# Performance work log

Measured on AMD Instinct MI355X. Metric: run time of the kernel, lower is better.

## Reference

```python
import jax, jax.numpy as jnp
import numpy as np
from jax import lax

EPS = 1e-5  # BatchNorm eps (inference-style BN with running stats)


def _bn(x, g, b, m, v):
    scale = g / jnp.sqrt(v + EPS)
    return x * scale[None, :, None, None] + (b - m * scale)[None, :, None, None]


def _conv1x1_bn(x, w, g, b, m, v):
    # ConvNormActivation(in_ch, out, k=1, activation=None) -> 1x1 conv (no bias) + BN
    y = jnp.einsum('bchw,oc->bohw', x, w)
    return _bn(y, g, b, m, v)


def _upsample_bilinear_ac(x, scale):
    # nn.Upsample(scale_factor=scale, mode='bilinear', align_corners=True)
    B, C, H, W = x.shape
    Ho, Wo = H * scale, W * scale

    def coords(n_in, n_out):
        s = jnp.arange(n_out, dtype=x.dtype) * ((n_in - 1) / (n_out - 1))
        i0 = jnp.clip(jnp.floor(s).astype(jnp.int32), 0, n_in - 2)
        t = s - i0.astype(x.dtype)
        return i0, t

    iy, ty = coords(H, Ho)
    ix, tx = coords(W, Wo)
    x = x[:, :, iy, :] * (1 - ty)[None, None, :, None] + x[:, :, iy + 1, :] * ty[None, None, :, None]
    x = x[:, :, :, ix] * (1 - tx) + x[:, :, :, ix + 1] * tx
    return x


def _dcnv2(x, off_w, off_b, w):
    # DCNv2: internal 3x3 conv -> 18 offsets (dy,dx per tap) + 9 sigmoid masks,
    # then modulated deformable 3x3 conv (stride 1, pad 1, no bias).
    B, C, H, W = x.shape
    K2 = 9
    om = lax.conv_general_dilated(x, off_w, (1, 1), ((1, 1), (1, 1)),
                                  dimension_numbers=('NCHW', 'OIHW', 'NCHW'))
    om = om + off_b[None, :, None, None]
    off = om[:, :2 * K2].reshape(B, K2, 2, H, W)          # (dy, dx) per kernel tap
    mask = jax.nn.sigmoid(om[:, 2 * K2:3 * K2])           # [B,9,H,W]

    ky, kx = jnp.meshgrid(jnp.arange(3), jnp.arange(3), indexing='ij')
    base_y = (jnp.arange(H)[None, :, None] + (ky.reshape(K2) - 1)[:, None, None]).astype(x.dtype)  # [9,H,1]
    base_x = (jnp.arange(W)[None, None, :] + (kx.reshape(K2) - 1)[:, None, None]).astype(x.dtype)  # [9,1,W]
    sy = base_y[None] + off[:, :, 0]                      # [B,9,H,W]
    sx = base_x[None] + off[:, :, 1]

    xf = x.reshape(B, C, H * W)
    y0 = jnp.floor(sy)
    x0 = jnp.floor(sx)
    val = jnp.zeros((B, C, K2, H, W), x.dtype)
    for dy in (0, 1):
        for dx in (0, 1):
            yy = y0 + dy
            xx = x0 + dx
            wgt = (1 - jnp.abs(sy - yy)) * (1 - jnp.abs(sx - xx))
            valid = (yy >= 0) & (yy <= H - 1) & (xx >= 0) & (xx <= W - 1)
            idx = jnp.clip(yy, 0, H - 1).astype(jnp.int32) * W + jnp.clip(xx, 0, W - 1).astype(jnp.int32)
            g = jnp.take_along_axis(xf, idx.reshape(B, 1, -1), axis=2).reshape(B, C, K2, H, W)
            val = val + g * (wgt * valid.astype(x.dtype))[:, None]
    val = val * mask[:, None]
    return jnp.einsum('bckhw,ock->bohw', val, w.reshape(w.shape[0], C, K2))


def _forward(f0, f1, f2, f3,
             w0, g0, b0, m0, v0, w1, g1, b1, m1, v1,
             w2, g2, b2, m2, v2, w3, g3, b3, m3, v3,
             off_w, off_b, dcn_w, gf, bf, mf, vf):
    x1 = _conv1x1_bn(f0, w0, g0, b0, m0, v0)
    x2 = _upsample_bilinear_ac(_conv1x1_bn(f1, w1, g1, b1, m1, v1), 2)
    x3 = _upsample_bilinear_ac(_conv1x1_bn(f2, w2, g2, b2, m2, v2), 4)
    x4 = _upsample_bilinear_ac(_conv1x1_bn(f3, w3, g3, b3, m3, v3), 8)
    x = jax.nn.relu(x1 + x2 + x3 + x4)
    y = _dcnv2(x, off_w, off_b, dcn_w)
    return jax.nn.relu(_bn(y, gf, bf, mf, vf))


def setup_inputs() -> dict:
    key = jax.random.key(0)
    ks = iter(jax.random.split(key, 64))

    def rn(shape, scale=1.0):
        return jax.random.normal(next(ks), shape, dtype=jnp.float32) * scale

    def ru(shape):
        return jax.random.uniform(next(ks), shape, dtype=jnp.float32)

    C = 64
    inp = {}
    inp['f0'] = rn((4, 64, 160, 160))
    inp['f1'] = rn((4, 128, 80, 80))
    inp['f2'] = rn((4, 256, 40, 40))
    inp['f3'] = rn((4, 512, 20, 20))
    for i, cin in enumerate([64, 128, 256, 512]):
        inp[f'w{i}'] = rn((C, cin), 1.0 / np.sqrt(cin))
        inp[f'g{i}'] = rn((C,))
        inp[f'b{i}'] = rn((C,))
        inp[f'm{i}'] = rn((C,))
        inp[f'v{i}'] = ru((C,))
    inp['off_w'] = rn((27, C, 3, 3), 0.01)   # small offsets, like post-training DCN
    inp['off_b'] = rn((27,), 0.01)
    inp['dcn_w'] = rn((C, C, 3, 3), 1.0 / np.sqrt(C * 9))
    inp['gf'] = rn((C,))
    inp['bf'] = rn((C,))
    inp['mf'] = rn((C,))
    inp['vf'] = ru((C,))
    return inp


def reference(f0, f1, f2, f3,
              w0, g0, b0, m0, v0, w1, g1, b1, m1, v1,
              w2, g2, b2, m2, v2, w3, g3, b3, m3, v3,
              off_w, off_b, dcn_w, gf, bf, mf, vf):
    return _forward(f0, f1, f2, f3,
                    w0, g0, b0, m0, v0, w1, g1, b1, m1, v1,
                    w2, g2, b2, m2, v2, w3, g3, b3, m3, v3,
                    off_w, off_b, dcn_w, gf, bf, mf, vf)
```

## Files before the change

kernel.cpp:

```cpp
#include <hip/hip_runtime.h>
#include <math.h>

#define EPSB 1e-5f

constexpr int B_ = 4;
constexpr int C_ = 64;
constexpr int H_ = 160;
constexpr int W_ = 160;
constexpr int HW_ = H_ * W_;

constexpr size_t X_OFF   = 0;
constexpr size_t Y1_OFF  = X_OFF  + (size_t)B_ * HW_ * 64;
constexpr size_t Y2_OFF  = Y1_OFF + (size_t)B_ * 6400 * 64;
constexpr size_t Y3_OFF  = Y2_OFF + (size_t)B_ * 1600 * 64;
constexpr size_t OM_OFF  = Y3_OFF + (size_t)B_ * 400 * 64;
constexpr size_t WR0_OFF = OM_OFF + (size_t)B_ * HW_ * 27;
constexpr size_t WTB_OFF = WR0_OFF + 4096;
constexpr size_t RWB_OFF = WTB_OFF + (9 * 64 * 72) / 2;
constexpr size_t SB_OFF  = RWB_OFF + (9 * 32 * 64) / 2;
constexpr size_t WR1_OFF = X_OFF + 0;
constexpr size_t WR2_OFF = X_OFF + 8192;
constexpr size_t WR3_OFF = X_OFF + 24576;

typedef short bf16x8 __attribute__((ext_vector_type(8)));
typedef float f32x4 __attribute__((ext_vector_type(4)));

static __device__ __forceinline__ unsigned short f2bf(float f) {
    unsigned int u = __float_as_uint(f);
    u += 0x7fff + ((u >> 16) & 1);
    return (unsigned short)(u >> 16);
}

__global__ __launch_bounds__(256) void prep_kernel(
    const float* __restrict__ g0, const float* __restrict__ b0, const float* __restrict__ m0, const float* __restrict__ v0,
    const float* __restrict__ g1, const float* __restrict__ b1, const float* __restrict__ m1, const float* __restrict__ v1,
    const float* __restrict__ g2, const float* __restrict__ b2, const float* __restrict__ m2, const float* __restrict__ v2,
    const float* __restrict__ g3, const float* __restrict__ b3, const float* __restrict__ m3, const float* __restrict__ v3,
    const float* __restrict__ gf, const float* __restrict__ bf, const float* __restrict__ mf, const float* __restrict__ vf,
    const float* __restrict__ w0, const float* __restrict__ w1, const float* __restrict__ w2, const float* __restrict__ w3,
    const float* __restrict__ dcn_w, const float* __restrict__ off_w,
    float* __restrict__ ws)
{
    int tid = blockIdx.x * 256 + threadIdx.x;
    if (tid < 320) {
        int j = tid >> 6, c = tid & 63;
        const float *g, *b, *m, *v;
        switch (j) {
            case 0: g = g0; b = b0; m = m0; v = v0; break;
            case 1: g = g1; b = b1; m = m1; v = v1; break;
            case 2: g = g2; b = b2; m = m2; v = v2; break;
            case 3: g = g3; b = b3; m = m3; v = v3; break;
            default: g = gf; b = bf; m = mf; v = vf; break;
        }
        float sc = g[c] * rsqrtf(v[c] + EPSB);
        ws[SB_OFF + j * 128 + c]      = sc;
        ws[SB_OFF + j * 128 + 64 + c] = b[c] - m[c] * sc;
        return;
    }
    int t = tid - 320;
    if (t < 4096) {
        int ci = t >> 6, o = t & 63;
        ws[WR0_OFF + t] = w0[o * 64 + ci];
        return;
    }
    t -= 4096;
    if (t < 9 * 64 * 72) {
        int k = t / 4608, r = t % 4608, o = r / 72, c = r % 72;
        float v = (c < 64) ? dcn_w[o * 576 + c * 9 + k] : 0.f;
        ((unsigned short*)(ws + WTB_OFF))[t] = f2bf(v);
        return;
    }
    t -= 9 * 64 * 72;
    if (t < 9 * 32 * 64) {
        int tap = t >> 11, r = t & 2047, o = r >> 6, ci = r & 63;
        float v = (o < 27) ? off_w[o * 576 + ci * 9 + tap] : 0.f;
        ((unsigned short*)(ws + RWB_OFF))[t] = f2bf(v);
        return;
    }
    t -= 9 * 32 * 64;
    if (t < 8192) {
        int ci = t >> 6, o = t & 63;
        ws[WR1_OFF + t] = w1[o * 128 + ci];
        return;
    }
    t -= 8192;
    if (t < 16384) {
        int ci = t >> 6, o = t & 63;
        ws[WR2_OFF + t] = w2[o * 256 + ci];
        return;
    }
    t -= 16384;
    if (t < 32768) {
        int ci = t >> 6, o = t & 63;
        ws[WR3_OFF + t] = w3[o * 512 + ci];
        return;
    }
}

__global__ __launch_bounds__(256) void conv_all_kernel(
    const float* __restrict__ f1in, const float* __restrict__ f2in, const float* __restrict__ f3in,
    float* __restrict__ ws)
{
    __shared__ float R0[64 * 65];
    __shared__ float R1[64 * 65];
    __shared__ float SBl[128];

    int blk = blockIdx.x;
    const float* fin; const float* wr; const float* sbg; float* yout;
    int Cin, hw, tile;
    if (blk < 400)      { fin = f1in; wr = ws + WR1_OFF; sbg = ws + SB_OFF + 128; yout = ws + Y1_OFF; Cin = 128; hw = 6400; tile = blk; }
    else if (blk < 500) { fin = f2in; wr = ws + WR2_OFF; sbg = ws + SB_OFF + 256; yout = ws + Y2_OFF; Cin = 256; hw = 1600; tile = blk - 400; }
    else                { fin = f3in; wr = ws + WR3_OFF; sbg = ws + SB_OFF + 384; yout = ws + Y3_OFF; Cin = 512; hw = 400;  tile = blk - 500; }

    int tid  = threadIdx.x;
    int lane = tid & 63;
    int wv   = __builtin_amdgcn_readfirstlane(tid >> 6);

    if (tid < 128) SBl[tid] = sbg[tid];

    int P = tile * 64 + lane;
    int b = P / hw;
    int p = P - b * hw;

    int cq = Cin >> 2;
    const float* fb = fin + ((size_t)b * Cin + (size_t)wv * cq) * hw + p;
    const float* wq = wr + (wv * cq) * 64;

    float acc[64];
#pragma unroll
    for (int o = 0; o < 64; o++) acc[o] = 0.f;

    for (int c0 = 0; c0 < cq; c0 += 8) {
        float fv[8];
#pragma unroll
        for (int j = 0; j < 8; j++) fv[j] = fb[(size_t)(c0 + j) * hw];
#pragma unroll
        for (int j = 0; j < 8; j++) {
            const float* wrow = wq + (c0 + j) * 64;
#pragma unroll
            for (int o = 0; o < 64; o++) acc[o] = fmaf(fv[j], wrow[o], acc[o]);
        }
    }

    if (wv == 2) {
#pragma unroll
        for (int o = 0; o < 64; o++) R0[lane * 65 + o] = acc[o];
    }
    if (wv == 3) {
#pragma unroll
        for (int o = 0; o < 64; o++) R1[lane * 65 + o] = acc[o];
    }
    __syncthreads();
    if (wv == 0) {
#pragma unroll
        for (int o = 0; o < 64; o++) acc[o] += R0[lane * 65 + o];
    }
    if (wv == 1) {
#pragma unroll
        for (int o = 0; o < 64; o++) acc[o] += R1[lane * 65 + o];
    }
    __syncthreads();
    if (wv == 1) {
#pragma unroll
        for (int o = 0; o < 64; o++) R0[lane * 65 + o] = acc[o];
    }
    __syncthreads();
    if (wv == 0) {
#pragma unroll
        for (int o = 0; o < 64; o++) {
            float v = acc[o] + R0[lane * 65 + o];
            R1[lane * 65 + o] = fmaf(v, SBl[o], SBl[64 + o]);
        }
    }
    __syncthreads();

#pragma unroll
    for (int it = 0; it < 16; it++) {
        int idx = it * 256 + tid;
        int px = idx >> 6, o = idx & 63;
        yout[(size_t)(tile * 64 + px) * 64 + o] = R1[px * 65 + o];
    }
}

__global__ __launch_bounds__(256) void fuse_kernel(const float* __restrict__ f0, float* __restrict__ ws)
{
    __shared__ float Ot[64 * 68];

    int tid = threadIdx.x;
    int blk = blockIdx.x;
    int xcd = blk & 7, slot = blk >> 3;
    int b = xcd >> 1;
    int t = (xcd & 1) * 200 + slot;
    int p0 = t * 64;
    int lane = tid & 63;
    int cb = __builtin_amdgcn_readfirstlane(tid >> 6);
    int p = p0 + lane;
    const float* wr0 = ws + WR0_OFF + cb * 16;
    const float* sb  = ws + SB_OFF;

    {
        float acc[16];
#pragma unroll
        for (int i = 0; i < 16; i++) acc[i] = 0.f;

        const float* f0b = f0 + (size_t)b * 64 * HW_ + p;
        for (int ci0 = 0; ci0 < 64; ci0 += 8) {
            float fv[8];
#pragma unroll
            for (int j = 0; j < 8; j++) fv[j] = f0b[(size_t)(ci0 + j) * HW_];
#pragma unroll
            for (int j = 0; j < 8; j++) {
                const float* wrow = wr0 + (ci0 + j) * 64;
#pragma unroll
                for (int i = 0; i < 16; i++) acc[i] = fmaf(fv[j], wrow[i], acc[i]);
            }
        }
        float* orow = Ot + lane * 68 + cb * 16;
#pragma unroll
        for (int i = 0; i < 16; i++) {
            int o = cb * 16 + i;
            orow[i] = fmaf(acc[i], sb[o], sb[64 + o]);
        }
    }
    __syncthreads();

    {
        int chunk = lane & 15, pxo = lane >> 4;
        float* xb = ws + X_OFF + ((size_t)b * HW_ + p0) * 64;
#pragma unroll
        for (int r = 0; r < 4; r++) {
            int gpx = cb * 16 + r * 4 + pxo;
            int gp = p0 + gpx;
            int h = gp / W_, w = gp % W_;

            float fy1 = h * (79.f / 159.f); int i1 = (int)fy1; if (i1 > 78) i1 = 78; float ty1 = fy1 - i1;
            float fx1 = w * (79.f / 159.f); int j1 = (int)fx1; if (j1 > 78) j1 = 78; float tx1 = fx1 - j1;
            const float* y1 = ws + Y1_OFF + ((size_t)b * 6400 + (size_t)(i1 * 80 + j1)) * 64 + chunk * 4;
            float fy2 = h * (39.f / 159.f); int i2 = (int)fy2; if (i2 > 38) i2 = 38; float ty2 = fy2 - i2;
            float fx2 = w * (39.f / 159.f); int j2 = (int)fx2; if (j2 > 38) j2 = 38; float tx2 = fx2 - j2;
            const float* y2 = ws + Y2_OFF + ((size_t)b * 1600 + (size_t)(i2 * 40 + j2)) * 64 + chunk * 4;
            float fy3 = h * (19.f / 159.f); int i3 = (int)fy3; if (i3 > 18) i3 = 18; float ty3 = fy3 - i3;
            float fx3 = w * (19.f / 159.f); int j3 = (int)fx3; if (j3 > 18) j3 = 18; float tx3 = fx3 - j3;
            const float* y3 = ws + Y3_OFF + ((size_t)b * 400 + (size_t)(i3 * 20 + j3)) * 64 + chunk * 4;

            f32x4 A[12];
            A[0]  = *(const f32x4*)(y1);
            A[1]  = *(const f32x4*)(y1 + 64);
            A[2]  = *(const f32x4*)(y1 + 80 * 64);
            A[3]  = *(const f32x4*)(y1 + 81 * 64);
            A[4]  = *(const f32x4*)(y2);
            A[5]  = *(const f32x4*)(y2 + 64);
            A[6]  = *(const f32x4*)(y2 + 40 * 64);
            A[7]  = *(const f32x4*)(y2 + 41 * 64);
            A[8]  = *(const f32x4*)(y3);
            A[9]  = *(const f32x4*)(y3 + 64);
            A[10] = *(const f32x4*)(y3 + 20 * 64);
            A[11] = *(const f32x4*)(y3 + 21 * 64);

            f32x4 v = *(const f32x4*)(Ot + gpx * 68 + chunk * 4);

            float w00, w01, w10, w11;
            w00 = (1.f - ty1) * (1.f - tx1); w01 = (1.f - ty1) * tx1; w10 = ty1 * (1.f - tx1); w11 = ty1 * tx1;
#pragma unroll
            for (int j = 0; j < 4; j++)
                v[j] += A[0][j] * w00 + A[1][j] * w01 + A[2][j] * w10 + A[3][j] * w11;
            w00 = (1.f - ty2) * (1.f - tx2); w01 = (1.f - ty2) * tx2; w10 = ty2 * (1.f - tx2); w11 = ty2 * tx2;
#pragma unroll
            for (int j = 0; j < 4; j++)
                v[j] += A[4][j] * w00 + A[5][j] * w01 + A[6][j] * w10 + A[7][j] * w11;
            w00 = (1.f - ty3) * (1.f - tx3); w01 = (1.f - ty3) * tx3; w10 = ty3 * (1.f - tx3); w11 = ty3 * tx3;
#pragma unroll
            for (int j = 0; j < 4; j++)
                v[j] += A[8][j] * w00 + A[9][j] * w01 + A[10][j] * w10 + A[11][j] * w11;

#pragma unroll
            for (int j = 0; j < 4; j++) v[j] = fmaxf(v[j], 0.f);
            *(f32x4*)(xb + (size_t)gpx * 64 + chunk * 4) = v;
        }
    }
}

__global__ __launch_bounds__(256, 4) void dcn_fused_kernel(const float* __restrict__ off_b,
                                                           float* __restrict__ ws, float* __restrict__ out)
{
    __shared__ __align__(16) unsigned short A_lds[2][64 * 72];
    __shared__ float OMs[64 * 27];

    int tid = threadIdx.x;
    int blk = blockIdx.x;
    int xcd = blk & 7, slot = blk >> 3;
    int b = xcd >> 1;
    int t = (xcd & 1) * 200 + slot;
    int p0 = t * 64;
    int lane = tid & 63, cb = tid >> 6;
    int px = lane;
    int p = p0 + px;
    int h = p / W_, w = p % W_;
    int mrow = lane & 15, quad = lane >> 4;
    int chunk = lane & 15, pxo = lane >> 4;

    const unsigned short* rwb = (const unsigned short*)(ws + RWB_OFF);
    const unsigned short* wtb = (const unsigned short*)(ws + WTB_OFF);
    const float* xb = ws + X_OFF + (size_t)b * HW_ * 64;
    const float* sb = ws + SB_OFF + 4 * 128;

    {
        f32x4 acc2[2];
        acc2[0] = (f32x4){0.f, 0.f, 0.f, 0.f};
        acc2[1] = (f32x4){0.f, 0.f, 0.f, 0.f};

        for (int kk = 0; kk < 9; kk += 2) {
#pragma unroll
            for (int u = 0; u < 2; u++) {
                int tap = kk + u;
                if (tap > 8) break;
                int dy = tap / 3 - 1, dx = tap % 3 - 1;
                int delta = dy * W_ + dx;
                int  pss[4];
                bool vlds[4];
#pragma unroll
                for (int r = 0; r < 4; r++) {
                    int gpx = cb * 16 + r * 4 + pxo;
                    int gp = p0 + gpx;
                    int gh = gp / W_, gw = gp % W_;
                    int yy = gh + dy, xx = gw + dx;
                    vlds[r] = (yy >= 0) && (yy < H_) && (xx >= 0) && (xx < W_);
                    int ps = gp + delta;
                    pss[r] = min(max(ps, 0), HW_ - 1);
                }
                f32x4 g[4];
#pragma unroll
                for (int r = 0; r < 4; r++)
                    g[r] = *(const f32x4*)(xb + (size_t)pss[r] * 64 + chunk * 4);
#pragma unroll
                for (int r = 0; r < 4; r++) {
                    int gpx = cb * 16 + r * 4 + pxo;
                    unsigned short pk[4];
#pragma unroll
                    for (int j = 0; j < 4; j++) pk[j] = vlds[r] ? f2bf(g[r][j]) : (unsigned short)0;
                    *(unsigned int*)(A_lds[u] + gpx * 72 + chunk * 4)     = ((unsigned int)pk[1] << 16) | pk[0];
                    *(unsigned int*)(A_lds[u] + gpx * 72 + chunk * 4 + 2) = ((unsigned int)pk[3] << 16) | pk[2];
                }
            }

#pragma unroll
            for (int u = 0; u < 2; u++) {
                int tap = kk + u;
                if (tap > 8) break;
                const unsigned short* Ab = A_lds[u] + (cb * 16 + mrow) * 72;
#pragma unroll
                for (int ks = 0; ks < 2; ks++) {
                    bf16x8 af = *(const bf16x8*)(Ab + ks * 32 + quad * 8);
#pragma unroll
                    for (int nt = 0; nt < 2; nt++) {
                        bf16x8 bf_ = *(const bf16x8*)(rwb + tap * 2048 + (nt * 16 + mrow) * 64 + ks * 32 + quad * 8);
                        acc2[nt] = __builtin_amdgcn_mfma_f32_16x16x32_bf16(af, bf_, acc2[nt], 0, 0, 0);
                    }
                }
            }
        }

        __syncthreads();
        float* Cl = (float*)A_lds;
#pragma unroll
        for (int nt = 0; nt < 2; nt++) {
            int o = nt * 16 + mrow;
            if (o < 27) {
                int pr = cb * 16 + quad * 4;
#pragma unroll
                for (int r = 0; r < 4; r++) Cl[(pr + r) * 28 + o] = acc2[nt][r];
            }
        }
        __syncthreads();

        for (int k = cb; k < 9; k += 4) {
            float ady = Cl[px * 28 + 2 * k]     + off_b[2 * k];
            float adx = Cl[px * 28 + 2 * k + 1] + off_b[2 * k + 1];
            float am  = Cl[px * 28 + 18 + k]    + off_b[18 + k];
            float sy = (float)(h + k / 3 - 1) + ady;
            float sx = (float)(w + k % 3 - 1) + adx;
            float mk = 1.f / (1.f + __expf(-am));
            OMs[px * 27 + 3 * k]     = sy;
            OMs[px * 27 + 3 * k + 1] = sx;
            OMs[px * 27 + 3 * k + 2] = mk;
        }
        __syncthreads();
    }

    f32x4 acc[4];
#pragma unroll
    for (int nt = 0; nt < 4; nt++) acc[nt] = (f32x4){0.f, 0.f, 0.f, 0.f};

    for (int kk = 0; kk < 9; kk += 2) {
#pragma unroll
        for (int u = 0; u < 2; u++) {
            int k = kk + u;
            if (k > 8) break;
#pragma unroll
            for (int rp = 0; rp < 2; rp++) {
                int   idxs[2][4];
                float wvs[2][4];
#pragma unroll
                for (int rr = 0; rr < 2; rr++) {
                    int r = rp * 2 + rr;
                    int gpx = cb * 16 + r * 4 + pxo;
                    float sy = OMs[gpx * 27 + 3 * k];
                    float sx = OMs[gpx * 27 + 3 * k + 1];
                    float mk = OMs[gpx * 27 + 3 * k + 2];
                    float y0f = floorf(sy), x0f = floorf(sx);
                    int y0 = (int)y0f, x0 = (int)x0f;
                    float ty = sy - y0f, tx = sx - x0f;
#pragma unroll
                    for (int cr = 0; cr < 4; cr++) {
                        int dy = cr >> 1, dx = cr & 1;
                        int yy = y0 + dy, xx = x0 + dx;
                        float wy = dy ? ty : 1.f - ty;
                        float wx = dx ? tx : 1.f - tx;
                        bool vld = (yy >= 0) && (yy < H_) && (xx >= 0) && (xx < W_);
                        int yc = min(max(yy, 0), H_ - 1);
                        int xc = min(max(xx, 0), W_ - 1);
                        idxs[rr][cr] = yc * W_ + xc;
                        wvs[rr][cr]  = vld ? wy * wx * mk : 0.f;
                    }
                }
                f32x4 g[2][4];
#pragma unroll
                for (int rr = 0; rr < 2; rr++)
#pragma unroll
                    for (int cr = 0; cr < 4; cr++)
                        g[rr][cr] = *(const f32x4*)(xb + (size_t)idxs[rr][cr] * 64 + chunk * 4);
#pragma unroll
                for (int rr = 0; rr < 2; rr++) {
                    int r = rp * 2 + rr;
                    int gpx = cb * 16 + r * 4 + pxo;
                    f32x4 v = (f32x4){0.f, 0.f, 0.f, 0.f};
#pragma unroll
                    for (int cr = 0; cr < 4; cr++) {
                        float wv = wvs[rr][cr];
#pragma unroll
                        for (int j = 0; j < 4; j++) v[j] = fmaf(g[rr][cr][j], wv, v[j]);
                    }
                    unsigned short pk[4];
#pragma unroll
                    for (int j = 0; j < 4; j++) pk[j] = f2bf(v[j]);
                    *(unsigned int*)(A_lds[u] + gpx * 72 + chunk * 4)     = ((unsigned int)pk[1] << 16) | pk[0];
                    *(unsigned int*)(A_lds[u] + gpx * 72 + chunk * 4 + 2) = ((unsigned int)pk[3] << 16) | pk[2];
                }
            }
        }

#pragma unroll
        for (int u = 0; u < 2; u++) {
            int k = kk + u;
            if (k > 8) break;
            const unsigned short* Ab = A_lds[u] + (cb * 16 + mrow) * 72;
#pragma unroll
            for (int ks = 0; ks < 2; ks++) {
                bf16x8 af = *(const bf16x8*)(Ab + ks * 32 + quad * 8);
#pragma unroll
                for (int nt = 0; nt < 4; nt++) {
                    bf16x8 bf_ = *(const bf16x8*)(wtb + k * 4608 + (nt * 16 + mrow) * 72 + ks * 32 + quad * 8);
                    acc[nt] = __builtin_amdgcn_mfma_f32_16x16x32_bf16(af, bf_, acc[nt], 0, 0, 0);
                }
            }
        }
    }

    __syncthreads();
    float* C_lds = (float*)A_lds;
#pragma unroll
    for (int nt = 0; nt < 4; nt++) {
        int o = nt * 16 + mrow;
        int pxb = cb * 16 + quad * 4;
#pragma unroll
        for (int r = 0; r < 4; r++) C_lds[o * 65 + pxb + r] = acc[nt][r];
    }
    __syncthreads();
#pragma unroll
    for (int i = 0; i < 16; i++) {
        int o = cb * 16 + i;
        float v = C_lds[o * 65 + lane];
        v = fmaf(v, sb[o], sb[64 + o]);
        out[((size_t)b * 64 + o) * HW_ + p0 + lane] = fmaxf(v, 0.f);
    }
}

extern "C" void kernel_launch(void* const* d_in, const int* in_sizes, int n_in,
                              void* d_out, int out_size, void* d_ws, size_t ws_size,
                              hipStream_t stream)
{
    const float* f0 = (const float*)d_in[0];
    const float* f1 = (const float*)d_in[1];
    const float* f2 = (const float*)d_in[2];
    const float* f3 = (const float*)d_in[3];
    const float* w0 = (const float*)d_in[4];
    const float* g0 = (const float*)d_in[5];
    const float* b0 = (const float*)d_in[6];
    const float* m0 = (const float*)d_in[7];
    const float* v0 = (const float*)d_in[8];
    const float* w1 = (const float*)d_in[9];
    const float* g1 = (const float*)d_in[10];
    const float* b1 = (const float*)d_in[11];
    const float* m1 = (const float*)d_in[12];
    const float* v1 = (const float*)d_in[13];
    const float* w2 = (const float*)d_in[14];
    const float* g2 = (const float*)d_in[15];
    const float* b2 = (const float*)d_in[16];
    const float* m2 = (const float*)d_in[17];
    const float* v2 = (const float*)d_in[18];
    const float* w3 = (const float*)d_in[19];
    const float* g3 = (const float*)d_in[20];
    const float* b3 = (const float*)d_in[21];
    const float* m3 = (const float*)d_in[22];
    const float* v3 = (const float*)d_in[23];
    const float* off_w = (const float*)d_in[24];
    const float* off_b = (const float*)d_in[25];
    const float* dcn_w = (const float*)d_in[26];
    const float* gf = (const float*)d_in[27];
    const float* bf = (const float*)d_in[28];
    const float* mf = (const float*)d_in[29];
    const float* vf = (const float*)d_in[30];

    float* ws  = (float*)d_ws;
    float* out = (float*)d_out;

    prep_kernel<<<dim3(476), dim3(256), 0, stream>>>(
        g0, b0, m0, v0, g1, b1, m1, v1, g2, b2, m2, v2, g3, b3, m3, v3,
        gf, bf, mf, vf, w0, w1, w2, w3, dcn_w, off_w, ws);

    conv_all_kernel<<<dim3(525), dim3(256), 0, stream>>>(f1, f2, f3, ws);

    fuse_kernel<<<dim3(1600), dim3(256), 0, stream>>>(f0, ws);

    dcn_fused_kernel<<<dim3(1600), dim3(256), 0, stream>>>(off_b, ws, out);
}
```

Baseline: 297.8 us.

## Store fused feature map in bf16 to halve gather traffic in DCN kernel

The fused feature map X is now written as bf16 by the upsample-add kernel instead of fp32. The DCN kernel's offset-conv gathers and deformable bilinear gathers read 8-byte bf16 vectors, which halves memory traffic and removes the float-to-bf16 conversions on the offset-conv path. The deformable path unpacks the bf16 values to fp32 for the bilinear weighting. Occupancy hint for the DCN kernel is raised from 4 to 6 blocks per CU. This adds rounding on the bilinear inputs, and the higher occupancy target may cause register spills.

```diff
diff --git a/kernel.cpp b/kernel.cpp
--- a/kernel.cpp
+++ b/kernel.cpp
@@ -24,6 +24,7 @@
 
 typedef short bf16x8 __attribute__((ext_vector_type(8)));
 typedef float f32x4 __attribute__((ext_vector_type(4)));
+typedef unsigned int u32x2 __attribute__((ext_vector_type(2)));
 
 static __device__ __forceinline__ unsigned short f2bf(float f) {
     unsigned int u = __float_as_uint(f);
@@ -226,7 +227,7 @@
 
     {
         int chunk = lane & 15, pxo = lane >> 4;
-        float* xb = ws + X_OFF + ((size_t)b * HW_ + p0) * 64;
+        unsigned short* xb = (unsigned short*)(ws + X_OFF) + ((size_t)b * HW_ + p0) * 64;
 #pragma unroll
         for (int r = 0; r < 4; r++) {
             int gpx = cb * 16 + r * 4 + pxo;
@@ -275,12 +276,14 @@
 
 #pragma unroll
             for (int j = 0; j < 4; j++) v[j] = fmaxf(v[j], 0.f);
-            *(f32x4*)(xb + (size_t)gpx * 64 + chunk * 4) = v;
+            unsigned int lo = ((unsigned int)f2bf(v[1]) << 16) | f2bf(v[0]);
+            unsigned int hi = ((unsigned int)f2bf(v[3]) << 16) | f2bf(v[2]);
+            *(u32x2*)(xb + (size_t)gpx * 64 + chunk * 4) = (u32x2){lo, hi};
         }
     }
 }
 
-__global__ __launch_bounds__(256, 4) void dcn_fused_kernel(const float* __restrict__ off_b,
+__global__ __launch_bounds__(256, 6) void dcn_fused_kernel(const float* __restrict__ off_b,
                                                            float* __restrict__ ws, float* __restrict__ out)
 {
     __shared__ __align__(16) unsigned short A_lds[2][64 * 72];
@@ -301,7 +304,7 @@
 
     const unsigned short* rwb = (const unsigned short*)(ws + RWB_OFF);
     const unsigned short* wtb = (const unsigned short*)(ws + WTB_OFF);
-    const float* xb = ws + X_OFF + (size_t)b * HW_ * 64;
+    const unsigned short* xbh = (const unsigned short*)(ws + X_OFF) + (size_t)b * HW_ * 64;
     const float* sb = ws + SB_OFF + 4 * 128;
 
     {
@@ -328,18 +331,17 @@
                     int ps = gp + delta;
                     pss[r] = min(max(ps, 0), HW_ - 1);
                 }
-                f32x4 g[4];
+                u32x2 g[4];
 #pragma unroll
                 for (int r = 0; r < 4; r++)
-                    g[r] = *(const f32x4*)(xb + (size_t)pss[r] * 64 + chunk * 4);
+                    g[r] = *(const u32x2*)(xbh + (size_t)pss[r] * 64 + chunk * 4);
 #pragma unroll
                 for (int r = 0; r < 4; r++) {
                     int gpx = cb * 16 + r * 4 + pxo;
-                    unsigned short pk[4];
-#pragma unroll
-                    for (int j = 0; j < 4; j++) pk[j] = vlds[r] ? f2bf(g[r][j]) : (unsigned short)0;
-                    *(unsigned int*)(A_lds[u] + gpx * 72 + chunk * 4)     = ((unsigned int)pk[1] << 16) | pk[0];
-                    *(unsigned int*)(A_lds[u] + gpx * 72 + chunk * 4 + 2) = ((unsigned int)pk[3] << 16) | pk[2];
+                    u32x2 gv;
+                    gv.x = vlds[r] ? g[r].x : 0u;
+                    gv.y = vlds[r] ? g[r].y : 0u;
+                    *(u32x2*)(A_lds[u] + gpx * 72 + chunk * 4) = gv;
                 }
             }
 
@@ -423,12 +425,12 @@
                         wvs[rr][cr]  = vld ? wy * wx * mk : 0.f;
                     }
                 }
-                f32x4 g[2][4];
+                u32x2 g[2][4];
 #pragma unroll
                 for (int rr = 0; rr < 2; rr++)
 #pragma unroll
                     for (int cr = 0; cr < 4; cr++)
-                        g[rr][cr] = *(const f32x4*)(xb + (size_t)idxs[rr][cr] * 64 + chunk * 4);
+                        g[rr][cr] = *(const u32x2*)(xbh + (size_t)idxs[rr][cr] * 64 + chunk * 4);
 #pragma unroll
                 for (int rr = 0; rr < 2; rr++) {
                     int r = rp * 2 + rr;
@@ -437,14 +439,18 @@
 #pragma unroll
                     for (int cr = 0; cr < 4; cr++) {
                         float wv = wvs[rr][cr];
-#pragma unroll
-                        for (int j = 0; j < 4; j++) v[j] = fmaf(g[rr][cr][j], wv, v[j]);
+                        float e0 = __uint_as_float(g[rr][cr].x << 16);
+                        float e1 = __uint_as_float(g[rr][cr].x & 0xffff0000u);
+                        float e2 = __uint_as_float(g[rr][cr].y << 16);
+                        float e3 = __uint_as_float(g[rr][cr].y & 0xffff0000u);
+                        v[0] = fmaf(e0, wv, v[0]);
+                        v[1] = fmaf(e1, wv, v[1]);
+                        v[2] = fmaf(e2, wv, v[2]);
+                        v[3] = fmaf(e3, wv, v[3]);
                     }
-                    unsigned short pk[4];
-#pragma unroll
-                    for (int j = 0; j < 4; j++) pk[j] = f2bf(v[j]);
-                    *(unsigned int*)(A_lds[u] + gpx * 72 + chunk * 4)     = ((unsigned int)pk[1] << 16) | pk[0];
-                    *(unsigned int*)(A_lds[u] + gpx * 72 + chunk * 4 + 2) = ((unsigned int)pk[3] << 16) | pk[2];
+                    unsigned int lo = ((unsigned int)f2bf(v[1]) << 16) | f2bf(v[0]);
+                    unsigned int hi = ((unsigned int)f2bf(v[3]) << 16) | f2bf(v[2]);
+                    *(u32x2*)(A_lds[u] + gpx * 72 + chunk * 4) = (u32x2){lo, hi};
                 }
             }
         }
```

After: 296.9 us. Within noise of the previous version (-0.3%).
